# Optimization experiments

Measured on AMD Instinct MI355X. Metric: run time of the kernel, lower is better.

Reference implementation:

```python
import jax, jax.numpy as jnp
import numpy as np

N = 4096            # data_length
T_IN, D_IN = 64, 128
F = 32 * 64         # target_length * output_dim


def setup_inputs() -> dict:
    key = jax.random.key(0)
    k1, k2, k3, k4 = jax.random.split(key, 4)
    xs = jax.random.normal(k1, (N, T_IN, D_IN), dtype=jnp.float32)
    W = jax.random.normal(k2, (T_IN * D_IN, F), dtype=jnp.float32) / np.sqrt(T_IN * D_IN)
    ys = jax.random.randint(k3, (N,), 0, 2, dtype=jnp.int32)  # {0,1} -> mapped to +-1 labels
    alphas = jax.random.normal(k4, (N,), dtype=jnp.float32)
    return {"xs": xs, "W": W, "ys": ys, "alphas": alphas}


def reference(xs, W, ys, alphas):
    gamma = 1.0 / F  # RBF bandwidth
    # encoder (stand-in for seq2seq): [N, T*D] @ [T*D, F] -> [N, F]
    X = xs.reshape(N, -1) @ W
    # pairwise squared distances via gram trick
    sq = jnp.sum(X * X, axis=-1)                       # [N]
    d2 = sq[:, None] + sq[None, :] - 2.0 * (X @ X.T)   # [N, N]
    d2 = jnp.maximum(d2, 0.0)
    K = jnp.exp(-gamma * d2)                           # RBF kernel matrix
    lab = (2 * ys - 1).astype(X.dtype)                 # +-1 labels
    G = (lab[:, None] * lab[None, :]) * K              # gram[i][j] = y_i y_j k(x_i, x_j)
    # 0.5 * alpha^T G alpha - sum(alpha)
    value = 0.5 * jnp.dot(alphas, G @ alphas) - jnp.sum(alphas)
    return value.reshape(1, 1)
```

## Files before the change

### kernel.cpp

```cpp
#include <hip/hip_runtime.h>
#include <hip/hip_bf16.h>

#define N_ROWS 4096
#define K_IN   8192
#define F_DIM  2048
#define GAMMA  (1.0f / 2048.0f)

typedef unsigned short u16;
typedef unsigned int   u32;
typedef unsigned char  u8;
typedef __attribute__((ext_vector_type(4))) int   i32x4;
typedef __attribute__((ext_vector_type(8))) int   i32x8;
typedef __attribute__((ext_vector_type(4))) float f32x4;
typedef __attribute__((ext_vector_type(2))) float f32x2;

__device__ __forceinline__ u32 pk4_fp8(float a, float b, float c, float d) {
  u32 u = 0;
  u = __builtin_amdgcn_cvt_pk_fp8_f32(a, b, u, false);
  u = __builtin_amdgcn_cvt_pk_fp8_f32(c, d, u, true);
  return u;
}
__device__ __forceinline__ u8 f8(float v) {
  return (u8)(__builtin_amdgcn_cvt_pk_fp8_f32(v, v, 0, false) & 0xff);
}

__device__ __forceinline__ void async16(const void* g, void* l) {
  __builtin_amdgcn_global_load_lds(
      (const __attribute__((address_space(1))) void*)g,
      (__attribute__((address_space(3))) void*)l, 16, 0, 0);
}


__global__ void convert_xs(const float4* __restrict__ in, u32* __restrict__ out, int n4) {
  int base = blockIdx.x * (blockDim.x * 4) + threadIdx.x;
#pragma unroll
  for (int k = 0; k < 4; ++k) {
    int i = base + k * 256;
    if (i < n4) {
      float4 v = in[i];
      out[i] = pk4_fp8(v.x, v.y, v.z, v.w);
    }
  }
}

__global__ void transpose_w(const float* __restrict__ W, u8* __restrict__ Wt) {
  __shared__ float tile[128][33];
  int k0 = blockIdx.x * 128;
  int f0 = blockIdx.y * 32;
  int tx = threadIdx.x, ty = threadIdx.y;
#pragma unroll
  for (int kk = 0; kk < 16; ++kk) {
    int k = kk * 8 + ty;
    tile[k][tx] = 64.0f * W[(size_t)(k0 + k) * F_DIM + f0 + tx];
  }
  __syncthreads();
#pragma unroll
  for (int ff = 0; ff < 4; ++ff) {
    int f = ff * 8 + ty;
    int kk = tx * 4;
    u32 p = pk4_fp8(tile[kk][f], tile[kk + 1][f], tile[kk + 2][f], tile[kk + 3][f]);
    *(u32*)(Wt + (size_t)(f0 + f) * K_IN + k0 + kk) = p;
  }
}

__global__ void prep(const float* __restrict__ alphas, const int* __restrict__ ys,
                     float* __restrict__ beta, float* __restrict__ out) {
  __shared__ float red[1024];
  int t = threadIdx.x;
  float s = 0.f;
  for (int i = t; i < N_ROWS; i += 1024) {
    float a = alphas[i];
    beta[i] = a * (float)(2 * ys[i] - 1);
    s += a;
  }
  red[t] = s;
  __syncthreads();
  for (int off = 512; off; off >>= 1) {
    if (t < off) red[t] += red[t + off];
    __syncthreads();
  }
  if (t == 0) out[0] = -red[0];
}

__global__ void row_sq(const u32* __restrict__ X, float* __restrict__ sq) {
  int wave = threadIdx.x >> 6, lane = threadIdx.x & 63;
  int row = blockIdx.x * 4 + wave;
  const uint4* xr = (const uint4*)(X + (size_t)row * (F_DIM / 4));
  float s = 0.f;
#pragma unroll
  for (int it = 0; it < 2; ++it) {
    uint4 v = xr[lane + it * 64];
    u32 w[4] = {v.x, v.y, v.z, v.w};
#pragma unroll
    for (int p = 0; p < 4; ++p) {
      f32x2 lo = __builtin_amdgcn_cvt_pk_f32_fp8(w[p], false);
      f32x2 hi = __builtin_amdgcn_cvt_pk_f32_fp8(w[p], true);
      s += lo[0] * lo[0] + lo[1] * lo[1] + hi[0] * hi[0] + hi[1] * hi[1];
    }
  }
#pragma unroll
  for (int off = 32; off; off >>= 1) s += __shfl_down(s, off);
  if (lane == 0) sq[row] = s;
}


template <int K>
__device__ __forceinline__ void gemm_tile_f8(const u8* __restrict__ A, const u8* __restrict__ Bt,
                                             int m0, int n0, u8* sA, u8* sB, int tid,
                                             int sclA, int sclB, f32x4 acc[4][4]) {
  const int lane = tid & 63;
  const int q = lane >> 4;
  const int r = lane & 15;
  const int wave = tid >> 6;
  const int wm = (wave >> 1) << 6;
  const int wn = (wave & 1) << 6;

  const f32x4 zero = {0.f, 0.f, 0.f, 0.f};
#pragma unroll
  for (int mt = 0; mt < 4; ++mt)
#pragma unroll
    for (int nt = 0; nt < 4; ++nt) acc[mt][nt] = zero;

  int rowS[4], colS[4], offS[4];
#pragma unroll
  for (int j = 0; j < 4; ++j) {
    int o = tid * 16 + j * 4096;
    int row = o >> 7;
    int cb = (o >> 4) & 7;
    rowS[j] = row;
    colS[j] = ((cb ^ (row & 7)) << 4);
    offS[j] = o;
  }

  for (int k0 = 0; k0 < K; k0 += 128) {
#pragma unroll
    for (int j = 0; j < 4; ++j) {
      async16(A + (size_t)(m0 + rowS[j]) * K + k0 + colS[j], sA + offS[j]);
      async16(Bt + (size_t)(n0 + rowS[j]) * K + k0 + colS[j], sB + offS[j]);
    }
    __syncthreads();

    i32x8 af[4], bg[4];
#pragma unroll
    for (int mt = 0; mt < 4; ++mt) {
      int m = wm + (mt << 4) + r;
      i32x4 lo = *(const i32x4*)(sA + m * 128 + ((((q << 1) | 0) ^ (m & 7)) << 4));
      i32x4 hi = *(const i32x4*)(sA + m * 128 + ((((q << 1) | 1) ^ (m & 7)) << 4));
      i32x8 f = {lo[0], lo[1], lo[2], lo[3], hi[0], hi[1], hi[2], hi[3]};
      af[mt] = f;
    }
#pragma unroll
    for (int nt = 0; nt < 4; ++nt) {
      int n = wn + (nt << 4) + r;
      i32x4 lo = *(const i32x4*)(sB + n * 128 + ((((q << 1) | 0) ^ (n & 7)) << 4));
      i32x4 hi = *(const i32x4*)(sB + n * 128 + ((((q << 1) | 1) ^ (n & 7)) << 4));
      i32x8 f = {lo[0], lo[1], lo[2], lo[3], hi[0], hi[1], hi[2], hi[3]};
      bg[nt] = f;
    }
#pragma unroll
    for (int mt = 0; mt < 4; ++mt)
#pragma unroll
      for (int nt = 0; nt < 4; ++nt)
        acc[mt][nt] = __builtin_amdgcn_mfma_scale_f32_16x16x128_f8f6f4(
            af[mt], bg[nt], acc[mt][nt], 0, 0, 0, sclA, 0, sclB);
    __syncthreads();
  }
}

__global__ __launch_bounds__(256, 3) void gemm_xw(const u8* __restrict__ A,
                                                  const u8* __restrict__ Bt,
                                                  u8* __restrict__ X) {
  __shared__ __align__(16) u8 sA[128 * 128];
  __shared__ __align__(16) u8 sB[128 * 128];
  const int tid = threadIdx.x;
  const int m0 = blockIdx.y << 7;
  const int n0 = blockIdx.x << 7;
  f32x4 acc[4][4];
  gemm_tile_f8<K_IN>(A, Bt, m0, n0, sA, sB, tid, 127, 121, acc);

  const int lane = tid & 63;
  const int q = lane >> 4;
  const int r = lane & 15;
  const int wave = tid >> 6;
  const int wm = (wave >> 1) << 6;
  const int wn = (wave & 1) << 6;
#pragma unroll
  for (int mt = 0; mt < 4; ++mt) {
#pragma unroll
    for (int nt = 0; nt < 4; ++nt) {
      int row = m0 + wm + (mt << 4) + (q << 2);
      int col = n0 + wn + (nt << 4) + r;
#pragma unroll
      for (int e = 0; e < 4; ++e)
        X[(size_t)(row + e) * F_DIM + col] = f8(acc[mt][nt][e]);
    }
  }
}

__global__ __launch_bounds__(256, 3) void gemm_kern(const u8* __restrict__ X,
                                                    const float* __restrict__ sq,
                                                    const float* __restrict__ beta,
                                                    float* __restrict__ out) {
  __shared__ __align__(16) u8 sA[128 * 128];
  __shared__ __align__(16) u8 sB[128 * 128];
  const int tid = threadIdx.x;
  int bid = blockIdx.x;
  int ib = 0;
  while (bid >= 32 - ib) { bid -= 32 - ib; ++ib; }
  const int jb = ib + bid;
  const int m0 = ib << 7;
  const int n0 = jb << 7;

  f32x4 acc[4][4];
  gemm_tile_f8<F_DIM>(X, X, m0, n0, sA, sB, tid, 127, 127, acc);

  const int lane = tid & 63;
  const int q = lane >> 4;
  const int r = lane & 15;
  const int wave = tid >> 6;
  const int wm = (wave >> 1) << 6;
  const int wn = (wave & 1) << 6;

  float sqj[4], bj[4];
#pragma unroll
  for (int nt = 0; nt < 4; ++nt) {
    int j = n0 + wn + (nt << 4) + r;
    sqj[nt] = sq[j];
    bj[nt] = beta[j];
  }
  float local = 0.f;
#pragma unroll
  for (int mt = 0; mt < 4; ++mt) {
#pragma unroll
    for (int e = 0; e < 4; ++e) {
      int i = m0 + wm + (mt << 4) + (q << 2) + e;
      float sqi = sq[i];
      float bi = beta[i];
#pragma unroll
      for (int nt = 0; nt < 4; ++nt) {
        float d2 = fmaxf(sqi + sqj[nt] - 2.f * acc[mt][nt][e], 0.f);
        local += bi * bj[nt] * __expf(-GAMMA * d2);
      }
    }
  }
  local *= (ib == jb) ? 0.5f : 1.0f;
#pragma unroll
  for (int off = 32; off; off >>= 1) local += __shfl_down(local, off);
  if (lane == 0) atomicAdd(out, local);
}


extern "C" void kernel_launch(void* const* d_in, const int* in_sizes, int n_in,
                              void* d_out, int out_size, void* d_ws, size_t ws_size,
                              hipStream_t stream) {
  const float* xs = (const float*)d_in[0];
  const float* W = (const float*)d_in[1];
  const int* ys = (const int*)d_in[2];
  const float* alphas = (const float*)d_in[3];
  float* out = (float*)d_out;

  char* ws = (char*)d_ws;
  u8* xs_f8 = (u8*)ws;
  u8* Wt_f8 = (u8*)(ws + 33554432);
  u8* X_f8  = (u8*)(ws + 50331648);
  float* sq   = (float*)(ws + 58720256);
  float* beta = (float*)(ws + 58736640);

  convert_xs<<<8192, 256, 0, stream>>>((const float4*)xs, (u32*)xs_f8,
                                       (N_ROWS * K_IN) / 4);
  dim3 tb(32, 8);
  dim3 tg(K_IN / 128, F_DIM / 32);
  transpose_w<<<tg, tb, 0, stream>>>(W, Wt_f8);
  prep<<<1, 1024, 0, stream>>>(alphas, ys, beta, out);

  dim3 g1(F_DIM / 128, N_ROWS / 128);
  gemm_xw<<<g1, 256, 0, stream>>>(xs_f8, Wt_f8, X_f8);
  row_sq<<<N_ROWS / 4, 256, 0, stream>>>((const u32*)X_f8, sq);
  gemm_kern<<<528, 256, 0, stream>>>(X_f8, sq, beta, out);
}
```

Before: 365.0 us.

## Rewrite XW GEMM with 256x128 tiles, triple-buffered async loads, interleaved MFMA

Replaces the shared tile routine in the encoder GEMM with a dedicated 512-thread kernel. It computes 256x128 output tiles and keeps three LDS stages filled with asynchronous global-to-LDS copies, issued two K-steps ahead. LDS fragment loads and prefetches are interleaved with MFMA groups using barriers, setprio and sched_barrier. Workgroups are remapped so neighbouring blocks share A/B panels across XCDs. The aim is to hide memory latency and raise MFMA utilisation, at the cost of about 144KB of LDS per block (one block per CU) and fragile hand-written waitcnt and barrier ordering.

```diff
diff --git a/kernel.cpp b/kernel.cpp
--- a/kernel.cpp
+++ b/kernel.cpp
@@ -167,16 +167,16 @@
   }
 }
 
-__global__ __launch_bounds__(256, 3) void gemm_xw(const u8* __restrict__ A,
+__global__ __launch_bounds__(512, 2) void gemm_xw(const u8* __restrict__ A,
                                                   const u8* __restrict__ Bt,
                                                   u8* __restrict__ X) {
-  __shared__ __align__(16) u8 sA[128 * 128];
-  __shared__ __align__(16) u8 sB[128 * 128];
+  __shared__ __align__(16) u8 sA[3][256 * 128];
+  __shared__ __align__(16) u8 sB[3][128 * 128];
   const int tid = threadIdx.x;
-  const int m0 = blockIdx.y << 7;
-  const int n0 = blockIdx.x << 7;
-  f32x4 acc[4][4];
-  gemm_tile_f8<K_IN>(A, Bt, m0, n0, sA, sB, tid, 127, 121, acc);
+  const int wg = blockIdx.x;
+  const int L = (wg & 7) * 32 + (wg >> 3);
+  const int m0 = (L & 15) << 8;
+  const int n0 = (L >> 4) << 7;
 
   const int lane = tid & 63;
   const int q = lane >> 4;
@@ -184,6 +184,110 @@
   const int wave = tid >> 6;
   const int wm = (wave >> 1) << 6;
   const int wn = (wave & 1) << 6;
+
+  const u8* gA[4]; int oA[4];
+  const u8* gB[2]; int oB[2];
+#pragma unroll
+  for (int j = 0; j < 4; ++j) {
+    int o = tid * 16 + j * 8192;
+    int row = o >> 7, cb = (o >> 4) & 7;
+    oA[j] = o;
+    gA[j] = A + (size_t)(m0 + row) * K_IN + ((cb ^ (row & 7)) << 4);
+  }
+#pragma unroll
+  for (int j = 0; j < 2; ++j) {
+    int o = tid * 16 + j * 8192;
+    int row = o >> 7, cb = (o >> 4) & 7;
+    oB[j] = o;
+    gB[j] = Bt + (size_t)(n0 + row) * K_IN + ((cb ^ (row & 7)) << 4);
+  }
+
+  const int cLo = (((q << 1) | 0) ^ (r & 7)) << 4;
+  const int cHi = (((q << 1) | 1) ^ (r & 7)) << 4;
+  const int aBase = (wm + r) << 7;
+  const int bBase = (wn + r) << 7;
+
+  f32x4 acc[4][4];
+  const f32x4 zero = {0.f, 0.f, 0.f, 0.f};
+#pragma unroll
+  for (int i = 0; i < 4; ++i)
+#pragma unroll
+    for (int j = 0; j < 4; ++j) acc[i][j] = zero;
+
+#pragma unroll
+  for (int j = 0; j < 4; ++j) async16(gA[j], &sA[0][oA[j]]);
+#pragma unroll
+  for (int j = 0; j < 2; ++j) async16(gB[j], &sB[0][oB[j]]);
+#pragma unroll
+  for (int j = 0; j < 4; ++j) async16(gA[j] + 128, &sA[1][oA[j]]);
+#pragma unroll
+  for (int j = 0; j < 2; ++j) async16(gB[j] + 128, &sB[1][oB[j]]);
+  asm volatile("s_waitcnt vmcnt(6)" ::: "memory");
+  __builtin_amdgcn_s_barrier();
+
+  i32x8 af0, af1, af2, af3, bg0, bg1, bg2, bg3;
+
+#define LDA(FR, MT, BUF) { \
+    const u8* b_ = &sA[BUF][aBase + (MT) * 2048]; \
+    i32x4 lo_ = *(const i32x4*)(b_ + cLo); \
+    i32x4 hi_ = *(const i32x4*)(b_ + cHi); \
+    FR = (i32x8){lo_[0], lo_[1], lo_[2], lo_[3], hi_[0], hi_[1], hi_[2], hi_[3]}; }
+#define LDB(FR, NT, BUF) { \
+    const u8* b_ = &sB[BUF][bBase + (NT) * 2048]; \
+    i32x4 lo_ = *(const i32x4*)(b_ + cLo); \
+    i32x4 hi_ = *(const i32x4*)(b_ + cHi); \
+    FR = (i32x8){lo_[0], lo_[1], lo_[2], lo_[3], hi_[0], hi_[1], hi_[2], hi_[3]}; }
+#define MFMA1(MT, NT, AF, BG) \
+    acc[MT][NT] = __builtin_amdgcn_mfma_scale_f32_16x16x128_f8f6f4( \
+        AF, BG, acc[MT][NT], 0, 0, 0, 127, 0, 121);
+
+  int cur = 0, nb = 2;
+  for (int kt = 0; kt < 64; ++kt) {
+    const bool st = (kt + 2 < 64);
+    const int k2 = (kt + 2) << 7;
+    LDA(af0, 0, cur) LDA(af1, 1, cur) LDB(bg0, 0, cur) LDB(bg1, 1, cur)
+    if (st) { async16(gA[0] + k2, &sA[nb][oA[0]]); async16(gA[1] + k2, &sA[nb][oA[1]]); }
+    __builtin_amdgcn_s_barrier();
+    asm volatile("s_waitcnt lgkmcnt(0)" ::: "memory");
+    __builtin_amdgcn_sched_barrier(0);
+    __builtin_amdgcn_s_setprio(1);
+    MFMA1(0, 0, af0, bg0) MFMA1(0, 1, af0, bg1) MFMA1(1, 0, af1, bg0) MFMA1(1, 1, af1, bg1)
+    __builtin_amdgcn_s_setprio(0);
+    __builtin_amdgcn_s_barrier();
+    LDA(af2, 2, cur) LDA(af3, 3, cur)
+    if (st) { async16(gA[2] + k2, &sA[nb][oA[2]]); async16(gA[3] + k2, &sA[nb][oA[3]]); }
+    __builtin_amdgcn_s_barrier();
+    asm volatile("s_waitcnt lgkmcnt(0)" ::: "memory");
+    __builtin_amdgcn_sched_barrier(0);
+    __builtin_amdgcn_s_setprio(1);
+    MFMA1(2, 0, af2, bg0) MFMA1(2, 1, af2, bg1) MFMA1(3, 0, af3, bg0) MFMA1(3, 1, af3, bg1)
+    __builtin_amdgcn_s_setprio(0);
+    __builtin_amdgcn_s_barrier();
+    LDB(bg2, 2, cur) LDB(bg3, 3, cur)
+    if (st) { async16(gB[0] + k2, &sB[nb][oB[0]]); async16(gB[1] + k2, &sB[nb][oB[1]]); }
+    __builtin_amdgcn_s_barrier();
+    asm volatile("s_waitcnt lgkmcnt(0)" ::: "memory");
+    __builtin_amdgcn_sched_barrier(0);
+    __builtin_amdgcn_s_setprio(1);
+    MFMA1(0, 2, af0, bg2) MFMA1(0, 3, af0, bg3) MFMA1(1, 2, af1, bg2) MFMA1(1, 3, af1, bg3)
+    __builtin_amdgcn_s_setprio(0);
+    __builtin_amdgcn_s_barrier();
+    __builtin_amdgcn_s_setprio(1);
+    MFMA1(2, 2, af2, bg2) MFMA1(2, 3, af2, bg3) MFMA1(3, 2, af3, bg2) MFMA1(3, 3, af3, bg3)
+    __builtin_amdgcn_s_setprio(0);
+    if (st) {
+      asm volatile("s_waitcnt vmcnt(6)" ::: "memory");
+    } else if (kt < 63) {
+      asm volatile("s_waitcnt vmcnt(0)" ::: "memory");
+    }
+    __builtin_amdgcn_s_barrier();
+    cur = (cur == 2) ? 0 : cur + 1;
+    nb  = (nb == 2) ? 0 : nb + 1;
+  }
+#undef LDA
+#undef LDB
+#undef MFMA1
+
 #pragma unroll
   for (int mt = 0; mt < 4; ++mt) {
 #pragma unroll
@@ -273,8 +377,7 @@
   transpose_w<<<tg, tb, 0, stream>>>(W, Wt_f8);
   prep<<<1, 1024, 0, stream>>>(alphas, ys, beta, out);
 
-  dim3 g1(F_DIM / 128, N_ROWS / 128);
-  gemm_xw<<<g1, 256, 0, stream>>>(xs_f8, Wt_f8, X_f8);
+  gemm_xw<<<256, 512, 0, stream>>>(xs_f8, Wt_f8, X_f8);
   row_sq<<<N_ROWS / 4, 256, 0, stream>>>((const u32*)X_f8, sq);
   gemm_kern<<<528, 256, 0, stream>>>(X_f8, sq, beta, out);
 }
```

New measurement: 371.1 us. No clear change (+1.7%).

## Pre-tile FP8 operands into MFMA fragment layout and split-K the XW GEMM

Applied to the files above, without the earlier changes.

The conversion kernels now write xs, W and X in a 16-row by 128-column tiled layout matching the MFMA fragment order. This lets the GEMMs load LDS with contiguous async copies and read fragments without swizzle arithmetic. gemm_xw becomes a 256x128 tile with 512 threads: two K-halves run in parallel and are reduced through LDS, and B is double-buffered. A block-index remap improves L2 locality. The cost is a more complex convert/store path and scattered byte stores in the epilogue.

```diff
diff --git a/kernel.cpp b/kernel.cpp
--- a/kernel.cpp
+++ b/kernel.cpp
@@ -14,6 +14,7 @@
 typedef __attribute__((ext_vector_type(4))) float f32x4;
 typedef __attribute__((ext_vector_type(2))) float f32x2;
 
+
 __device__ __forceinline__ u32 pk4_fp8(float a, float b, float c, float d) {
   u32 u = 0;
   u = __builtin_amdgcn_cvt_pk_fp8_f32(a, b, u, false);
@@ -31,16 +32,28 @@
 }
 
 
-__global__ void convert_xs(const float4* __restrict__ in, u32* __restrict__ out, int n4) {
-  int base = blockIdx.x * (blockDim.x * 4) + threadIdx.x;
-#pragma unroll
-  for (int k = 0; k < 4; ++k) {
-    int i = base + k * 256;
-    if (i < n4) {
-      float4 v = in[i];
-      out[i] = pk4_fp8(v.x, v.y, v.z, v.w);
-    }
-  }
+__global__ void convert_xs(const float* __restrict__ xs, u8* __restrict__ out) {
+  __shared__ float t16[16][132];
+  const int bid = blockIdx.x;
+  const int rt = bid >> 6, kt = bid & 63;
+  const int tid = threadIdx.x;
+  const float* src = xs + (size_t)rt * 16 * K_IN + kt * 128;
+#pragma unroll
+  for (int j = 0; j < 2; ++j) {
+    int i = tid + j * 256;
+    int row = i >> 5, c4 = (i & 31) << 2;
+    float4 v = *(const float4*)(src + (size_t)row * K_IN + c4);
+    t16[row][c4 + 0] = v.x; t16[row][c4 + 1] = v.y;
+    t16[row][c4 + 2] = v.z; t16[row][c4 + 3] = v.w;
+  }
+  __syncthreads();
+  const int cw = tid >> 1, part = tid & 1;
+  const int h = cw >> 6, l = cw & 63, q = l >> 4, rr = l & 15;
+  const float* p = &t16[rr][q * 32 + h * 16 + part * 8];
+  u32 u0 = pk4_fp8(p[0], p[1], p[2], p[3]);
+  u32 u1 = pk4_fp8(p[4], p[5], p[6], p[7]);
+  uint2 st = {u0, u1};
+  *(uint2*)(out + ((size_t)(rt * 64 + kt) << 11) + cw * 16 + part * 8) = st;
 }
 
 __global__ void transpose_w(const float* __restrict__ W, u8* __restrict__ Wt) {
@@ -54,12 +67,15 @@
     tile[k][tx] = 64.0f * W[(size_t)(k0 + k) * F_DIM + f0 + tx];
   }
   __syncthreads();
+  const int kt = k0 >> 7;
 #pragma unroll
   for (int ff = 0; ff < 4; ++ff) {
     int f = ff * 8 + ty;
     int kk = tx * 4;
     u32 p = pk4_fp8(tile[kk][f], tile[kk + 1][f], tile[kk + 2][f], tile[kk + 3][f]);
-    *(u32*)(Wt + (size_t)(f0 + f) * K_IN + k0 + kk) = p;
+    int rt = (f0 + f) >> 4, rr = (f0 + f) & 15;
+    int q = kk >> 5, hh = (kk >> 4) & 1, b = kk & 15;
+    *(u32*)(Wt + ((size_t)(rt * 64 + kt) << 11) + hh * 1024 + (q * 16 + rr) * 16 + b) = p;
   }
 }
 
@@ -85,11 +101,14 @@
 __global__ void row_sq(const u32* __restrict__ X, float* __restrict__ sq) {
   int wave = threadIdx.x >> 6, lane = threadIdx.x & 63;
   int row = blockIdx.x * 4 + wave;
-  const uint4* xr = (const uint4*)(X + (size_t)row * (F_DIM / 4));
+  const u8* base = (const u8*)X + ((size_t)(row >> 4) << 15);
+  const int rr = row & 15;
   float s = 0.f;
 #pragma unroll
   for (int it = 0; it < 2; ++it) {
-    uint4 v = xr[lane + it * 64];
+    int c = lane + it * 64;
+    int kt = c >> 3, q = (c >> 1) & 3, h = c & 1;
+    uint4 v = *(const uint4*)(base + kt * 2048 + h * 1024 + (q * 16 + rr) * 16);
     u32 w[4] = {v.x, v.y, v.z, v.w};
 #pragma unroll
     for (int p = 0; p < 4; ++p) {
@@ -103,97 +122,165 @@
   if (lane == 0) sq[row] = s;
 }
 
-
-template <int K>
-__device__ __forceinline__ void gemm_tile_f8(const u8* __restrict__ A, const u8* __restrict__ Bt,
-                                             int m0, int n0, u8* sA, u8* sB, int tid,
-                                             int sclA, int sclB, f32x4 acc[4][4]) {
+__global__ __launch_bounds__(512, 2) void gemm_xw(const u8* __restrict__ A,
+                                                  const u8* __restrict__ Bt,
+                                                  u8* __restrict__ X) {
+  __shared__ __align__(16) u8 smem[131072];
+  const int tid = threadIdx.x;
+  const int wg = blockIdx.x;
+  const int L = (wg & 7) * 32 + (wg >> 3);
+  const int m0 = (L & 15) << 8;
+  const int n0 = (L >> 4) << 7;
+
   const int lane = tid & 63;
-  const int q = lane >> 4;
-  const int r = lane & 15;
   const int wave = tid >> 6;
-  const int wm = (wave >> 1) << 6;
-  const int wn = (wave & 1) << 6;
-
+  const int kh = wave >> 2;
+  const int w2 = wave & 3;
+  const int wm = (w2 >> 1) << 7;
+  const int wn = (w2 & 1) << 6;
+  const int t = tid & 255;
+
+  u8* sA  = smem + kh * 65536;
+  u8* sB0 = sA + 32768;
+  u8* sB1 = sB0 + 16384;
+
+  const u8* pA = A  + (size_t)((m0 >> 4) + (t >> 7)) * 131072 + (t & 127) * 16;
+  const u8* pB = Bt + (size_t)((n0 >> 4) + (t >> 7)) * 131072 + (t & 127) * 16;
+  const int oT = t * 16;
+
+  f32x4 acc[8][4];
   const f32x4 zero = {0.f, 0.f, 0.f, 0.f};
 #pragma unroll
+  for (int i = 0; i < 8; ++i)
+#pragma unroll
+    for (int j = 0; j < 4; ++j) acc[i][j] = zero;
+
+#define STAGE_A(KT) { _Pragma("unroll") for (int j_ = 0; j_ < 8; ++j_) \
+    async16(pA + (size_t)j_ * 262144 + (size_t)(KT) * 2048, sA + oT + j_ * 4096); }
+#define STAGE_B(BUF, KT) { _Pragma("unroll") for (int j_ = 0; j_ < 4; ++j_) \
+    async16(pB + (size_t)j_ * 262144 + (size_t)(KT) * 2048, (BUF) + oT + j_ * 4096); }
+#define MFMA1(MT, NT, AF, BG) \
+    acc[MT][NT] = __builtin_amdgcn_mfma_scale_f32_16x16x128_f8f6f4( \
+        AF, BG, acc[MT][NT], 0, 0, 0, 127, 0, 121);
+
+  const int kbase = kh * 32;
+  STAGE_A(kbase)
+  STAGE_B(sB0, kbase)
+  __syncthreads();
+
+  const int aB = lane * 16;
+  const int sa0 = wm >> 4;
+  const int sb0i = wn >> 4;
+
+  for (int it = 0; it < 32; ++it) {
+    const int kt = kbase + it;
+    u8* sBc = (it & 1) ? sB1 : sB0;
+    u8* sBn = (it & 1) ? sB0 : sB1;
+
+    i32x8 af[8];
+#pragma unroll
+    for (int mt = 0; mt < 8; ++mt) {
+      const u8* b_ = sA + (sa0 + mt) * 2048 + aB;
+      i32x4 lo = *(const i32x4*)(b_);
+      i32x4 hi = *(const i32x4*)(b_ + 1024);
+      af[mt] = (i32x8){lo[0], lo[1], lo[2], lo[3], hi[0], hi[1], hi[2], hi[3]};
+    }
+    __syncthreads();
+
+    if (it < 31) { STAGE_A(kt + 1) STAGE_B(sBn, kt + 1) }
+#pragma unroll
+    for (int nt = 0; nt < 4; ++nt) {
+      const u8* b_ = sBc + (sb0i + nt) * 2048 + aB;
+      i32x4 lo = *(const i32x4*)(b_);
+      i32x4 hi = *(const i32x4*)(b_ + 1024);
+      i32x8 bg = (i32x8){lo[0], lo[1], lo[2], lo[3], hi[0], hi[1], hi[2], hi[3]};
+      MFMA1(0, nt, af[0], bg) MFMA1(1, nt, af[1], bg)
+      MFMA1(2, nt, af[2], bg) MFMA1(3, nt, af[3], bg)
+      MFMA1(4, nt, af[4], bg) MFMA1(5, nt, af[5], bg)
+      MFMA1(6, nt, af[6], bg) MFMA1(7, nt, af[7], bg)
+    }
+    __syncthreads();
+  }
+#undef STAGE_A
+#undef STAGE_B
+#undef MFMA1
+
+  __syncthreads();
+  float* red = (float*)smem;
+  if (kh == 1) {
+#pragma unroll
+    for (int mt = 0; mt < 8; ++mt)
+#pragma unroll
+      for (int nt = 0; nt < 4; ++nt)
+        *(f32x4*)(red + ((size_t)t * 32 + mt * 4 + nt) * 4) = acc[mt][nt];
+  }
+  __syncthreads();
+  if (kh == 0) {
+    const int q = lane >> 4, r = lane & 15;
+    const int qq0 = wn >> 5;
+#pragma unroll
+    for (int mt = 0; mt < 8; ++mt) {
+#pragma unroll
+      for (int nt = 0; nt < 4; ++nt) {
+        f32x4 v = acc[mt][nt] + *(const f32x4*)(red + ((size_t)t * 32 + mt * 4 + nt) * 4);
+        const int rt = (m0 >> 4) + (wm >> 4) + mt;
+        const int qq = qq0 + (nt >> 1);
+        const int hh = nt & 1;
+        u8* dst = X + (size_t)rt * 32768 + (size_t)(n0 >> 7) * 2048 + hh * 1024 + r;
+#pragma unroll
+        for (int e = 0; e < 4; ++e)
+          dst[(qq * 16 + ((q << 2) + e)) * 16] = f8(v[e]);
+      }
+    }
+  }
+}
+
+__device__ __forceinline__ void gemm_tile_x(const u8* __restrict__ X, int m0, int n0,
+                                            u8* sA, u8* sB, int tid, f32x4 acc[4][4]) {
+  const int lane = tid & 63;
+  const int wave = tid >> 6;
+  const f32x4 zero = {0.f, 0.f, 0.f, 0.f};
+#pragma unroll
   for (int mt = 0; mt < 4; ++mt)
 #pragma unroll
     for (int nt = 0; nt < 4; ++nt) acc[mt][nt] = zero;
 
-  int rowS[4], colS[4], offS[4];
-#pragma unroll
-  for (int j = 0; j < 4; ++j) {
-    int o = tid * 16 + j * 4096;
-    int row = o >> 7;
-    int cb = (o >> 4) & 7;
-    rowS[j] = row;
-    colS[j] = ((cb ^ (row & 7)) << 4);
-    offS[j] = o;
-  }
-
-  for (int k0 = 0; k0 < K; k0 += 128) {
+  const u8* pA = X + (size_t)((m0 >> 4) + (tid >> 7)) * 32768 + (tid & 127) * 16;
+  const u8* pB = X + (size_t)((n0 >> 4) + (tid >> 7)) * 32768 + (tid & 127) * 16;
+  const int oT = tid * 16;
+  const int aB = lane * 16;
+  const int sa0 = (wave >> 1) * 4, sb0 = (wave & 1) * 4;
+
+  for (int kt = 0; kt < 16; ++kt) {
 #pragma unroll
     for (int j = 0; j < 4; ++j) {
-      async16(A + (size_t)(m0 + rowS[j]) * K + k0 + colS[j], sA + offS[j]);
-      async16(Bt + (size_t)(n0 + rowS[j]) * K + k0 + colS[j], sB + offS[j]);
+      async16(pA + (size_t)j * 65536 + kt * 2048, sA + oT + j * 4096);
+      async16(pB + (size_t)j * 65536 + kt * 2048, sB + oT + j * 4096);
     }
     __syncthreads();
 
     i32x8 af[4], bg[4];
 #pragma unroll
     for (int mt = 0; mt < 4; ++mt) {
-      int m = wm + (mt << 4) + r;
-      i32x4 lo = *(const i32x4*)(sA + m * 128 + ((((q << 1) | 0) ^ (m & 7)) << 4));
-      i32x4 hi = *(const i32x4*)(sA + m * 128 + ((((q << 1) | 1) ^ (m & 7)) << 4));
-      i32x8 f = {lo[0], lo[1], lo[2], lo[3], hi[0], hi[1], hi[2], hi[3]};
-      af[mt] = f;
+      const u8* b_ = sA + (sa0 + mt) * 2048 + aB;
+      i32x4 lo = *(const i32x4*)(b_);
+      i32x4 hi = *(const i32x4*)(b_ + 1024);
+      af[mt] = (i32x8){lo[0], lo[1], lo[2], lo[3], hi[0], hi[1], hi[2], hi[3]};
     }
 #pragma unroll
     for (int nt = 0; nt < 4; ++nt) {
-      int n = wn + (nt << 4) + r;
-      i32x4 lo = *(const i32x4*)(sB + n * 128 + ((((q << 1) | 0) ^ (n & 7)) << 4));
-      i32x4 hi = *(const i32x4*)(sB + n * 128 + ((((q << 1) | 1) ^ (n & 7)) << 4));
-      i32x8 f = {lo[0], lo[1], lo[2], lo[3], hi[0], hi[1], hi[2], hi[3]};
-      bg[nt] = f;
+      const u8* b_ = sB + (sb0 + nt) * 2048 + aB;
+      i32x4 lo = *(const i32x4*)(b_);
+      i32x4 hi = *(const i32x4*)(b_ + 1024);
+      bg[nt] = (i32x8){lo[0], lo[1], lo[2], lo[3], hi[0], hi[1], hi[2], hi[3]};
     }
 #pragma unroll
     for (int mt = 0; mt < 4; ++mt)
 #pragma unroll
       for (int nt = 0; nt < 4; ++nt)
         acc[mt][nt] = __builtin_amdgcn_mfma_scale_f32_16x16x128_f8f6f4(
-            af[mt], bg[nt], acc[mt][nt], 0, 0, 0, sclA, 0, sclB);
-    __syncthreads();
-  }
-}
-
-__global__ __launch_bounds__(256, 3) void gemm_xw(const u8* __restrict__ A,
-                                                  const u8* __restrict__ Bt,
-                                                  u8* __restrict__ X) {
-  __shared__ __align__(16) u8 sA[128 * 128];
-  __shared__ __align__(16) u8 sB[128 * 128];
-  const int tid = threadIdx.x;
-  const int m0 = blockIdx.y << 7;
-  const int n0 = blockIdx.x << 7;
-  f32x4 acc[4][4];
-  gemm_tile_f8<K_IN>(A, Bt, m0, n0, sA, sB, tid, 127, 121, acc);
-
-  const int lane = tid & 63;
-  const int q = lane >> 4;
-  const int r = lane & 15;
-  const int wave = tid >> 6;
-  const int wm = (wave >> 1) << 6;
-  const int wn = (wave & 1) << 6;
-#pragma unroll
-  for (int mt = 0; mt < 4; ++mt) {
-#pragma unroll
-    for (int nt = 0; nt < 4; ++nt) {
-      int row = m0 + wm + (mt << 4) + (q << 2);
-      int col = n0 + wn + (nt << 4) + r;
-#pragma unroll
-      for (int e = 0; e < 4; ++e)
-        X[(size_t)(row + e) * F_DIM + col] = f8(acc[mt][nt][e]);
-    }
+            af[mt], bg[nt], acc[mt][nt], 0, 0, 0, 127, 0, 127);
+    __syncthreads();
   }
 }
 
@@ -212,7 +299,7 @@
   const int n0 = jb << 7;
 
   f32x4 acc[4][4];
-  gemm_tile_f8<F_DIM>(X, X, m0, n0, sA, sB, tid, 127, 127, acc);
+  gemm_tile_x(X, m0, n0, sA, sB, tid, acc);
 
   const int lane = tid & 63;
   const int q = lane >> 4;
@@ -266,15 +353,13 @@
   float* sq   = (float*)(ws + 58720256);
   float* beta = (float*)(ws + 58736640);
 
-  convert_xs<<<8192, 256, 0, stream>>>((const float4*)xs, (u32*)xs_f8,
-                                       (N_ROWS * K_IN) / 4);
+  convert_xs<<<16384, 256, 0, stream>>>(xs, xs_f8);
   dim3 tb(32, 8);
   dim3 tg(K_IN / 128, F_DIM / 32);
   transpose_w<<<tg, tb, 0, stream>>>(W, Wt_f8);
   prep<<<1, 1024, 0, stream>>>(alphas, ys, beta, out);
 
-  dim3 g1(F_DIM / 128, N_ROWS / 128);
-  gemm_xw<<<g1, 256, 0, stream>>>(xs_f8, Wt_f8, X_f8);
+  gemm_xw<<<256, 512, 0, stream>>>(xs_f8, Wt_f8, X_f8);
   row_sq<<<N_ROWS / 4, 256, 0, stream>>>((const u32*)X_f8, sq);
   gemm_kern<<<528, 256, 0, stream>>>(X_f8, sq, beta, out);
 }
```

Result: no change. 358.8 us (-1.7%).
